# Kernel tuning notes

Hardware: AMD Instinct MI355X
Metric: run time of the kernel (lower is better)

Reference implementation:

```python
import jax, jax.numpy as jnp
import numpy as np

N = 16      # manifold_dim
H = 128     # hidden_dim
B = 256     # batch
EPS = 1e-6


def setup_inputs() -> dict:
    key = jax.random.key(0)
    ks = jax.random.split(key, 14)
    def w(k, shape):
        fan_in = shape[0]
        return jax.random.uniform(k, shape, jnp.float32, -1.0, 1.0) / np.sqrt(fan_in)
    return {
        "points": jax.random.normal(ks[0], (B, N), jnp.float32),
        # metric network: N -> H -> N*N
        "mW1": w(ks[1], (N, H)), "mb1": jnp.zeros((H,), jnp.float32),
        "mW2": w(ks[2], (H, N * N)), "mb2": jnp.zeros((N * N,), jnp.float32),
        # christoffel network: 3 -> H -> 1
        "cW1": w(ks[3], (3, H)), "cb1": jnp.zeros((H,), jnp.float32),
        "cW2": w(ks[4], (H, 1)), "cb2": jnp.zeros((1,), jnp.float32),
        # ricci network: 4N -> 2H -> N*N
        "rW1": w(ks[5], (4 * N, 2 * H)), "rb1": jnp.zeros((2 * H,), jnp.float32),
        "rW2": w(ks[6], (2 * H, N * N)), "rb2": jnp.zeros((N * N,), jnp.float32),
    }


def reference(points, mW1, mb1, mW2, mb2, cW1, cb1, cW2, cb2, rW1, rb1, rW2, rb2):
    b = points.shape[0]
    n = N
    # ---- metric: (b, n, n) ----
    mh = jax.nn.relu(points @ mW1 + mb1)
    metric = (mh @ mW2 + mb2).reshape(b, n, n)
    metric = metric + EPS * jnp.eye(n, dtype=metric.dtype)
    metric = 0.5 * (metric + jnp.swapaxes(metric, -2, -1))

    # ---- christoffel: vectorized over all (i,j,k) triples ----
    # inputs per triple: [metric_ij, metric_jk, metric_ki]
    m_ij = jnp.broadcast_to(metric[:, :, :, None], (b, n, n, n))
    m_jk = jnp.broadcast_to(metric[:, None, :, :], (b, n, n, n))
    mT = jnp.swapaxes(metric, -2, -1)  # mT[b,i,k] = metric[b,k,i]
    m_ki = jnp.broadcast_to(mT[:, :, None, :], (b, n, n, n))
    ch_in = jnp.stack([m_ij, m_jk, m_ki], axis=-1)        # (b,n,n,n,3)
    ch_h = jnp.tanh(ch_in @ cW1 + cb1)                    # (b,n,n,n,H)
    christoffel = (ch_h @ cW2 + cb2)[..., 0]              # (b,n,n,n)

    # ---- ricci: vectorized over all (i,j) pairs ----
    p_b = jnp.broadcast_to(points[:, None, None, :], (b, n, n, n))
    m_i = jnp.broadcast_to(metric[:, :, None, :], (b, n, n, n))
    m_j = jnp.broadcast_to(metric[:, None, :, :], (b, n, n, n))
    r_in = jnp.concatenate([p_b, m_i, m_j, christoffel], axis=-1)  # (b,n,n,4n)
    r_h = jax.nn.relu(r_in @ rW1 + rb1)                   # (b,n,n,2H)
    r_out = (r_h @ rW2 + rb2).reshape(b, n, n, n, n)      # (b,i,j,n,n)
    r_out = 0.5 * (r_out + jnp.swapaxes(r_out, -1, -2))
    ricci = r_out.sum(axis=(1, 2)) / (n * n)              # (b,n,n)
    return ricci
```

## Files before the change

kernel.cpp:

```cpp
#include <hip/hip_runtime.h>
#include <hip/hip_bf16.h>

#define NDIM 16
#define HDIM 128
#define BATCH 256
#define EPS_D 1e-6f

__global__ __launch_bounds__(256) void metric_proj_kernel(
    const float* __restrict__ points,
    const float* __restrict__ mW1, const float* __restrict__ mb1,
    const float* __restrict__ mW2, const float* __restrict__ mb2,
    const float* __restrict__ rW1, const float* __restrict__ rb1,
    float* __restrict__ metric,
    float* __restrict__ A1, float* __restrict__ Mi, float* __restrict__ Mj,
    float* __restrict__ G) {
  int b = blockIdx.x;
  int t = threadIdx.x;
  __shared__ float p[16];
  __shared__ float mh[128];
  __shared__ float raw[256];
  __shared__ float M[256];
  G[b * 256 + t] = 0.f;
  if (t < 16) p[t] = points[b * 16 + t];
  __syncthreads();
  if (t < 128) {
    float acc = mb1[t];
#pragma unroll
    for (int k = 0; k < 16; ++k) acc = fmaf(p[k], mW1[k * 128 + t], acc);
    mh[t] = fmaxf(acc, 0.f);
  }
  __syncthreads();
  {
    float acc = mb2[t];
#pragma unroll 8
    for (int h = 0; h < 128; ++h) acc = fmaf(mh[h], mW2[h * 256 + t], acc);
    raw[t] = acc;
  }
  __syncthreads();
  {
    int i = t >> 4, j = t & 15;
    float v = 0.5f * (raw[i * 16 + j] + raw[j * 16 + i]);
    if (i == j) v += EPS_D;
    M[t] = v;
    metric[b * 256 + t] = v;
  }
  __syncthreads();
  {
    int h = t;
    float wB[16], wC[16];
#pragma unroll
    for (int c = 0; c < 16; ++c) {
      wB[c] = rW1[(16 + c) * 256 + h];
      wC[c] = rW1[(32 + c) * 256 + h];
    }
    float a = rb1[h];
#pragma unroll
    for (int r = 0; r < 16; ++r) a = fmaf(p[r], rW1[r * 256 + h], a);
    A1[b * 256 + h] = a;
#pragma unroll 2
    for (int i = 0; i < 16; ++i) {
      float mi = 0.f, mj = 0.f;
#pragma unroll
      for (int c = 0; c < 16; ++c) {
        float m = M[i * 16 + c];
        mi = fmaf(m, wB[c], mi);
        mj = fmaf(m, wC[c], mj);
      }
      Mi[(b * 16 + i) * 256 + h] = mi;
      Mj[(b * 16 + i) * 256 + h] = mj;
    }
  }
}

__global__ __launch_bounds__(256, 4) void chr_kernel(
    const float* __restrict__ metric,
    const float* __restrict__ cW1, const float* __restrict__ cb1,
    const float* __restrict__ cW2, const float* __restrict__ cb2,
    const float* __restrict__ rW1,
    const float* __restrict__ A1, const float* __restrict__ Mi,
    const float* __restrict__ Mj,
    float* __restrict__ G) {
  int blk = blockIdx.x;
  int b = blk >> 2, g = blk & 3;
  int t = threadIdx.x;
  int w = t >> 6, l = t & 63;
  int i = g * 4 + w;
  int bi = b * 16 + i;
  __shared__ float M[256];
  __shared__ float4 z[128];
  __shared__ float4 w2p[32];
  __shared__ float4 ch4[256];
  float* chf = (float*)ch4;
  M[t] = metric[b * 256 + t];
  if (t < 128) {
    const float S = 2.8853900817779268f;
    z[t] = make_float4(S * cW1[t], S * cW1[128 + t], S * cW1[256 + t],
                       S * cb1[t]);
  } else {
    ((float*)w2p)[t - 128] = cW2[t - 128];
  }
  __syncthreads();

  {
    float x0[4], x1[4], x2[4], acc[4];
    float c2 = cb2[0];
#pragma unroll
    for (int m = 0; m < 4; ++m) {
      int jk = l + 64 * m;
      int j = jk >> 4, k = jk & 15;
      x0[m] = M[i * 16 + j];
      x1[m] = M[j * 16 + k];
      x2[m] = M[k * 16 + i];
      acc[m] = c2;
    }
    for (int h = 0; h < 128; h += 4) {
      float4 W2 = w2p[h >> 2];
      float w2u[4] = {W2.x, W2.y, W2.z, W2.w};
#pragma unroll
      for (int u = 0; u < 4; ++u) {
        float4 Q = z[h + u];
#pragma unroll
        for (int m = 0; m < 4; ++m) {
          float pre = fmaf(x0[m], Q.x, fmaf(x1[m], Q.y, fmaf(x2[m], Q.z, Q.w)));
          float e = __builtin_amdgcn_exp2f(pre);
          float r = __builtin_amdgcn_rcpf(e + 1.f);
          acc[m] = fmaf(w2u[u], fmaf(-2.f, r, 1.f), acc[m]);
        }
      }
    }
#pragma unroll
    for (int m = 0; m < 4; ++m) chf[w * 256 + l + 64 * m] = acc[m];
  }

  {
    float rc[4][16];
#pragma unroll
    for (int kk = 0; kk < 16; ++kk) {
#pragma unroll
      for (int m = 0; m < 4; ++m)
        rc[m][kk] = rW1[(48 + kk) * 256 + l + 64 * m];
    }
    float base[4], hacc[4];
#pragma unroll
    for (int m = 0; m < 4; ++m) {
      int h = l + 64 * m;
      base[m] = A1[b * 256 + h] + Mi[bi * 256 + h];
      hacc[m] = 0.f;
    }
    for (int jj = 0; jj < 16; ++jj) {
      float4 c0 = ch4[w * 64 + jj * 4 + 0];
      float4 c1 = ch4[w * 64 + jj * 4 + 1];
      float4 c2v = ch4[w * 64 + jj * 4 + 2];
      float4 c3 = ch4[w * 64 + jj * 4 + 3];
      float cc[16] = {c0.x, c0.y, c0.z, c0.w, c1.x, c1.y, c1.z, c1.w,
                      c2v.x, c2v.y, c2v.z, c2v.w, c3.x, c3.y, c3.z, c3.w};
#pragma unroll
      for (int m = 0; m < 4; ++m) {
        float cp = 0.f;
#pragma unroll
        for (int kk = 0; kk < 16; ++kk) cp = fmaf(cc[kk], rc[m][kk], cp);
        float mj = Mj[(b * 16 + jj) * 256 + l + 64 * m];
        hacc[m] += fmaxf(base[m] + mj + cp, 0.f);
      }
    }
#pragma unroll
    for (int m = 0; m < 4; ++m)
      atomicAdd(&G[b * 256 + l + 64 * m], hacc[m]);
  }
}

__global__ __launch_bounds__(256) void final_kernel(
    const float* __restrict__ G,
    const float* __restrict__ rW2, const float* __restrict__ rb2,
    float* __restrict__ out) {
  int b = blockIdx.x;
  int t = threadIdx.x;
  __shared__ float4 Gs[64];
  __shared__ float T[256];
  if (t < 64) Gs[t] = ((const float4*)(G + b * 256))[t];
  __syncthreads();
  float acc = 256.f * rb2[t];
#pragma unroll 4
  for (int h4 = 0; h4 < 64; ++h4) {
    float4 gg = Gs[h4];
    acc = fmaf(gg.x, rW2[(h4 * 4 + 0) * 256 + t], acc);
    acc = fmaf(gg.y, rW2[(h4 * 4 + 1) * 256 + t], acc);
    acc = fmaf(gg.z, rW2[(h4 * 4 + 2) * 256 + t], acc);
    acc = fmaf(gg.w, rW2[(h4 * 4 + 3) * 256 + t], acc);
  }
  T[t] = acc * (1.f / 256.f);
  __syncthreads();
  int k = t >> 4, lcol = t & 15;
  out[b * 256 + t] = 0.5f * (T[k * 16 + lcol] + T[lcol * 16 + k]);
}

extern "C" void kernel_launch(void* const* d_in, const int* in_sizes, int n_in,
                              void* d_out, int out_size, void* d_ws, size_t ws_size,
                              hipStream_t stream) {
  const float* points = (const float*)d_in[0];
  const float* mW1 = (const float*)d_in[1];
  const float* mb1 = (const float*)d_in[2];
  const float* mW2 = (const float*)d_in[3];
  const float* mb2 = (const float*)d_in[4];
  const float* cW1 = (const float*)d_in[5];
  const float* cb1 = (const float*)d_in[6];
  const float* cW2 = (const float*)d_in[7];
  const float* cb2 = (const float*)d_in[8];
  const float* rW1 = (const float*)d_in[9];
  const float* rb1 = (const float*)d_in[10];
  const float* rW2 = (const float*)d_in[11];
  const float* rb2 = (const float*)d_in[12];
  float* out = (float*)d_out;

  float* ws = (float*)d_ws;
  float* metric = ws;
  float* A1 = metric + 65536;
  float* Mi = A1 + 65536;
  float* Mj = Mi + 1048576;
  float* G = Mj + 1048576;

  metric_proj_kernel<<<BATCH, 256, 0, stream>>>(points, mW1, mb1, mW2, mb2,
                                                rW1, rb1, metric, A1, Mi, Mj, G);
  chr_kernel<<<BATCH * 4, 256, 0, stream>>>(metric, cW1, cb1, cW2, cb2, rW1,
                                            A1, Mi, Mj, G);
  final_kernel<<<BATCH, 256, 0, stream>>>(G, rW2, rb2, out);
}
```

Measured before the change: 143.6 us.

## Split christoffel kernel to one block per (b,i) with packed float2 math

Changes chr_kernel from 1024 blocks of 256 threads (4 i-rows each) to 4096 blocks of 128 threads, each handling one (b,i) row with two elements per thread. The arithmetic uses float2 vector types so the compiler can emit packed FMA instructions, while exp2 and rcp stay scalar. The aim is more parallel blocks, less per-thread register pressure and higher FMA throughput. In exchange the shared-memory weight setup is redone per block four times as often, and there are four times as many atomic adds to G.

```diff
diff --git a/kernel.cpp b/kernel.cpp
--- a/kernel.cpp
+++ b/kernel.cpp
@@ -5,6 +5,14 @@
 #define HDIM 128
 #define BATCH 256
 #define EPS_D 1e-6f
+
+typedef float v2f __attribute__((ext_vector_type(2)));
+static __device__ __forceinline__ v2f v2(float a, float b) {
+  v2f r; r.x = a; r.y = b; return r;
+}
+static __device__ __forceinline__ v2f splat(float a) {
+  v2f r; r.x = a; r.y = a; return r;
+}
 
 __global__ __launch_bounds__(256) void metric_proj_kernel(
     const float* __restrict__ points,
@@ -72,7 +80,7 @@
   }
 }
 
-__global__ __launch_bounds__(256, 4) void chr_kernel(
+__global__ __launch_bounds__(128, 6) void chr_kernel(
     const float* __restrict__ metric,
     const float* __restrict__ cW1, const float* __restrict__ cb1,
     const float* __restrict__ cW2, const float* __restrict__ cb2,
@@ -80,92 +88,88 @@
     const float* __restrict__ A1, const float* __restrict__ Mi,
     const float* __restrict__ Mj,
     float* __restrict__ G) {
-  int blk = blockIdx.x;
-  int b = blk >> 2, g = blk & 3;
+  int bi = blockIdx.x;
+  int b = bi >> 4, i = bi & 15;
   int t = threadIdx.x;
   int w = t >> 6, l = t & 63;
-  int i = g * 4 + w;
-  int bi = b * 16 + i;
   __shared__ float M[256];
   __shared__ float4 z[128];
   __shared__ float4 w2p[32];
-  __shared__ float4 ch4[256];
+  __shared__ float4 ch4[64];
   float* chf = (float*)ch4;
   M[t] = metric[b * 256 + t];
-  if (t < 128) {
+  M[t + 128] = metric[b * 256 + t + 128];
+  {
     const float S = 2.8853900817779268f;
     z[t] = make_float4(S * cW1[t], S * cW1[128 + t], S * cW1[256 + t],
                        S * cb1[t]);
-  } else {
-    ((float*)w2p)[t - 128] = cW2[t - 128];
-  }
-  __syncthreads();
-
-  {
-    float x0[4], x1[4], x2[4], acc[4];
-    float c2 = cb2[0];
-#pragma unroll
-    for (int m = 0; m < 4; ++m) {
-      int jk = l + 64 * m;
-      int j = jk >> 4, k = jk & 15;
-      x0[m] = M[i * 16 + j];
-      x1[m] = M[j * 16 + k];
-      x2[m] = M[k * 16 + i];
-      acc[m] = c2;
-    }
-    for (int h = 0; h < 128; h += 4) {
-      float4 W2 = w2p[h >> 2];
+    ((float*)w2p)[t] = cW2[t];
+  }
+  __syncthreads();
+
+  {
+    int jk0 = w * 128 + l, jk1 = jk0 + 64;
+    int j0 = jk0 >> 4, k0 = jk0 & 15;
+    int j1 = jk1 >> 4, k1 = jk1 & 15;
+    v2f x0 = v2(M[i * 16 + j0], M[i * 16 + j1]);
+    v2f x1 = v2(M[j0 * 16 + k0], M[j1 * 16 + k1]);
+    v2f x2 = v2(M[k0 * 16 + i], M[k1 * 16 + i]);
+    v2f acc = splat(cb2[0]);
+    for (int hq = 0; hq < 32; ++hq) {
+      float4 W2 = w2p[hq];
       float w2u[4] = {W2.x, W2.y, W2.z, W2.w};
 #pragma unroll
       for (int u = 0; u < 4; ++u) {
-        float4 Q = z[h + u];
-#pragma unroll
-        for (int m = 0; m < 4; ++m) {
-          float pre = fmaf(x0[m], Q.x, fmaf(x1[m], Q.y, fmaf(x2[m], Q.z, Q.w)));
-          float e = __builtin_amdgcn_exp2f(pre);
-          float r = __builtin_amdgcn_rcpf(e + 1.f);
-          acc[m] = fmaf(w2u[u], fmaf(-2.f, r, 1.f), acc[m]);
-        }
+        float4 Q = z[hq * 4 + u];
+        v2f pre = __builtin_elementwise_fma(
+            x0, splat(Q.x),
+            __builtin_elementwise_fma(
+                x1, splat(Q.y),
+                __builtin_elementwise_fma(x2, splat(Q.z), splat(Q.w))));
+        v2f e;
+        e.x = __builtin_amdgcn_exp2f(pre.x);
+        e.y = __builtin_amdgcn_exp2f(pre.y);
+        v2f ep = e + splat(1.f);
+        v2f r;
+        r.x = __builtin_amdgcn_rcpf(ep.x);
+        r.y = __builtin_amdgcn_rcpf(ep.y);
+        v2f th = __builtin_elementwise_fma(splat(-2.f), r, splat(1.f));
+        acc = __builtin_elementwise_fma(th, splat(w2u[u]), acc);
       }
     }
-#pragma unroll
-    for (int m = 0; m < 4; ++m) chf[w * 256 + l + 64 * m] = acc[m];
-  }
-
-  {
-    float rc[4][16];
-#pragma unroll
-    for (int kk = 0; kk < 16; ++kk) {
-#pragma unroll
-      for (int m = 0; m < 4; ++m)
-        rc[m][kk] = rW1[(48 + kk) * 256 + l + 64 * m];
-    }
-    float base[4], hacc[4];
-#pragma unroll
-    for (int m = 0; m < 4; ++m) {
-      int h = l + 64 * m;
-      base[m] = A1[b * 256 + h] + Mi[bi * 256 + h];
-      hacc[m] = 0.f;
-    }
+    chf[jk0] = acc.x;
+    chf[jk1] = acc.y;
+  }
+  __syncthreads();
+
+  {
+    int h0 = w * 128 + l, h1 = h0 + 64;
+    v2f rc2[16];
+#pragma unroll
+    for (int kk = 0; kk < 16; ++kk)
+      rc2[kk] = v2(rW1[(48 + kk) * 256 + h0], rW1[(48 + kk) * 256 + h1]);
+    v2f base = v2(A1[b * 256 + h0] + Mi[bi * 256 + h0],
+                  A1[b * 256 + h1] + Mi[bi * 256 + h1]);
+    v2f hacc = splat(0.f);
     for (int jj = 0; jj < 16; ++jj) {
-      float4 c0 = ch4[w * 64 + jj * 4 + 0];
-      float4 c1 = ch4[w * 64 + jj * 4 + 1];
-      float4 c2v = ch4[w * 64 + jj * 4 + 2];
-      float4 c3 = ch4[w * 64 + jj * 4 + 3];
+      float4 c0 = ch4[jj * 4 + 0];
+      float4 c1 = ch4[jj * 4 + 1];
+      float4 c2v = ch4[jj * 4 + 2];
+      float4 c3 = ch4[jj * 4 + 3];
+      v2f mj = v2(Mj[(b * 16 + jj) * 256 + h0], Mj[(b * 16 + jj) * 256 + h1]);
+      v2f cp = base + mj;
       float cc[16] = {c0.x, c0.y, c0.z, c0.w, c1.x, c1.y, c1.z, c1.w,
                       c2v.x, c2v.y, c2v.z, c2v.w, c3.x, c3.y, c3.z, c3.w};
 #pragma unroll
-      for (int m = 0; m < 4; ++m) {
-        float cp = 0.f;
-#pragma unroll
-        for (int kk = 0; kk < 16; ++kk) cp = fmaf(cc[kk], rc[m][kk], cp);
-        float mj = Mj[(b * 16 + jj) * 256 + l + 64 * m];
-        hacc[m] += fmaxf(base[m] + mj + cp, 0.f);
-      }
-    }
-#pragma unroll
-    for (int m = 0; m < 4; ++m)
-      atomicAdd(&G[b * 256 + l + 64 * m], hacc[m]);
+      for (int kk = 0; kk < 16; ++kk)
+        cp = __builtin_elementwise_fma(splat(cc[kk]), rc2[kk], cp);
+      v2f rl;
+      rl.x = fmaxf(cp.x, 0.f);
+      rl.y = fmaxf(cp.y, 0.f);
+      hacc += rl;
+    }
+    atomicAdd(&G[b * 256 + h0], hacc.x);
+    atomicAdd(&G[b * 256 + h1], hacc.y);
   }
 }
 
@@ -221,7 +225,7 @@
 
   metric_proj_kernel<<<BATCH, 256, 0, stream>>>(points, mW1, mb1, mW2, mb2,
                                                 rW1, rb1, metric, A1, Mi, Mj, G);
-  chr_kernel<<<BATCH * 4, 256, 0, stream>>>(metric, cW1, cb1, cW2, cb2, rW1,
-                                            A1, Mi, Mj, G);
+  chr_kernel<<<BATCH * NDIM, 128, 0, stream>>>(metric, cW1, cb1, cW2, cb2, rW1,
+                                               A1, Mi, Mj, G);
   final_kernel<<<BATCH, 256, 0, stream>>>(G, rW2, rb2, out);
 }
```

Result: faster. 135.7 us (-5.5%).

## Replace exp/rcp tanh with packed rational polynomial and vectorize via v2f packed FMA

Applied to the files above, without the earlier changes.

The christoffel hidden-layer tanh, previously computed with exp2 plus reciprocal, becomes a clamped odd rational polynomial evaluated with two-wide float vectors so the compiler can emit packed FP32 FMA instructions. The four per-lane denominators are inverted with a single reciprocal using a shared-product trick. The ricci first-layer accumulation is also rewritten with packed FMAs. The aim is to cut transcendental-unit work and halve the VALU instruction count, at the cost of more FMAs per element and slightly different tanh accuracy near the clamp.

```diff
diff --git a/kernel.cpp b/kernel.cpp
--- a/kernel.cpp
+++ b/kernel.cpp
@@ -5,6 +5,30 @@
 #define HDIM 128
 #define BATCH 256
 #define EPS_D 1e-6f
+
+typedef float v2f __attribute__((ext_vector_type(2)));
+static __device__ __forceinline__ v2f v2(float a, float b) {
+  v2f r; r.x = a; r.y = b; return r;
+}
+static __device__ __forceinline__ v2f splat(float a) {
+  v2f r; r.x = a; r.y = a; return r;
+}
+#define VFMA(a, b, c) __builtin_elementwise_fma((a), (b), (c))
+#define VMIN(a, b) __builtin_elementwise_min((a), (b))
+#define VMAX(a, b) __builtin_elementwise_max((a), (b))
+
+#define TCLAMP 7.99881172180175781f
+#define CA1 4.89352455891786e-03f
+#define CA3 6.37261928875436e-04f
+#define CA5 1.48572235717979e-05f
+#define CA7 5.12229709037114e-08f
+#define CA9 -8.60467152213735e-11f
+#define CA11 2.00018790482477e-13f
+#define CA13 -2.76076847742355e-16f
+#define CB0 4.89352518554385e-03f
+#define CB2 2.26843463243900e-03f
+#define CB4 1.18534705686654e-04f
+#define CB6 1.19825839466702e-06f
 
 __global__ __launch_bounds__(256) void metric_proj_kernel(
     const float* __restrict__ points,
@@ -88,65 +112,75 @@
   int bi = b * 16 + i;
   __shared__ float M[256];
   __shared__ float4 z[128];
-  __shared__ float4 w2p[32];
+  __shared__ float w2s[128];
   __shared__ float4 ch4[256];
   float* chf = (float*)ch4;
   M[t] = metric[b * 256 + t];
   if (t < 128) {
-    const float S = 2.8853900817779268f;
-    z[t] = make_float4(S * cW1[t], S * cW1[128 + t], S * cW1[256 + t],
-                       S * cb1[t]);
-  } else {
-    ((float*)w2p)[t - 128] = cW2[t - 128];
-  }
-  __syncthreads();
-
-  {
-    float x0[4], x1[4], x2[4], acc[4];
+    z[t] = make_float4(cW1[t], cW1[128 + t], cW1[256 + t], cb1[t]);
+    w2s[t] = cW2[t];
+  }
+  __syncthreads();
+
+  {
+    int j0 = l >> 4, k0 = l & 15;
+    v2f x0A = v2(M[i * 16 + j0], M[i * 16 + j0 + 8]);
+    v2f x0B = v2(M[i * 16 + j0 + 4], M[i * 16 + j0 + 12]);
+    v2f x1A = v2(M[j0 * 16 + k0], M[(j0 + 8) * 16 + k0]);
+    v2f x1B = v2(M[(j0 + 4) * 16 + k0], M[(j0 + 12) * 16 + k0]);
+    float x2s = M[k0 * 16 + i];
     float c2 = cb2[0];
-#pragma unroll
-    for (int m = 0; m < 4; ++m) {
-      int jk = l + 64 * m;
-      int j = jk >> 4, k = jk & 15;
-      x0[m] = M[i * 16 + j];
-      x1[m] = M[j * 16 + k];
-      x2[m] = M[k * 16 + i];
-      acc[m] = c2;
-    }
-    for (int h = 0; h < 128; h += 4) {
-      float4 W2 = w2p[h >> 2];
-      float w2u[4] = {W2.x, W2.y, W2.z, W2.w};
-#pragma unroll
-      for (int u = 0; u < 4; ++u) {
-        float4 Q = z[h + u];
-#pragma unroll
-        for (int m = 0; m < 4; ++m) {
-          float pre = fmaf(x0[m], Q.x, fmaf(x1[m], Q.y, fmaf(x2[m], Q.z, Q.w)));
-          float e = __builtin_amdgcn_exp2f(pre);
-          float r = __builtin_amdgcn_rcpf(e + 1.f);
-          acc[m] = fmaf(w2u[u], fmaf(-2.f, r, 1.f), acc[m]);
-        }
-      }
-    }
-#pragma unroll
-    for (int m = 0; m < 4; ++m) chf[w * 256 + l + 64 * m] = acc[m];
-  }
-
-  {
-    float rc[4][16];
+    v2f accA = splat(c2), accB = splat(c2);
+#pragma unroll 2
+    for (int h = 0; h < 128; ++h) {
+      float4 Q = z[h];
+      float w2h = w2s[h];
+      float bb = fmaf(x2s, Q.z, Q.w);
+      v2f preA = VFMA(x0A, splat(Q.x), VFMA(x1A, splat(Q.y), splat(bb)));
+      v2f preB = VFMA(x0B, splat(Q.x), VFMA(x1B, splat(Q.y), splat(bb)));
+      v2f tA = VMAX(VMIN(preA, splat(TCLAMP)), splat(-TCLAMP));
+      v2f tB = VMAX(VMIN(preB, splat(TCLAMP)), splat(-TCLAMP));
+      v2f sA = tA * tA, sB = tB * tB;
+      v2f pA = VFMA(sA, splat(CA13), splat(CA11));
+      v2f pB = VFMA(sB, splat(CA13), splat(CA11));
+      pA = VFMA(sA, pA, splat(CA9));  pB = VFMA(sB, pB, splat(CA9));
+      pA = VFMA(sA, pA, splat(CA7));  pB = VFMA(sB, pB, splat(CA7));
+      pA = VFMA(sA, pA, splat(CA5));  pB = VFMA(sB, pB, splat(CA5));
+      pA = VFMA(sA, pA, splat(CA3));  pB = VFMA(sB, pB, splat(CA3));
+      pA = VFMA(sA, pA, splat(CA1));  pB = VFMA(sB, pB, splat(CA1));
+      pA = pA * tA;  pB = pB * tB;
+      v2f qA = VFMA(sA, splat(CB6), splat(CB4));
+      v2f qB = VFMA(sB, splat(CB6), splat(CB4));
+      qA = VFMA(sA, qA, splat(CB2));  qB = VFMA(sB, qB, splat(CB2));
+      qA = VFMA(sA, qA, splat(CB0));  qB = VFMA(sB, qB, splat(CB0));
+      v2f prod = qA * qB;
+      float r = __builtin_amdgcn_rcpf(prod.x * prod.y);
+      v2f u = splat(r) * v2(prod.y, prod.x);
+      v2f rcpA = u * qB;
+      v2f rcpB = u * qA;
+      accA = VFMA(pA * rcpA, splat(w2h), accA);
+      accB = VFMA(pB * rcpB, splat(w2h), accB);
+    }
+    chf[w * 256 + l] = accA.x;
+    chf[w * 256 + l + 64] = accB.x;
+    chf[w * 256 + l + 128] = accA.y;
+    chf[w * 256 + l + 192] = accB.y;
+  }
+
+  {
+    int h0 = l, h1 = l + 64, h2 = l + 128, h3 = l + 192;
+    v2f rcA[16], rcB[16];
 #pragma unroll
     for (int kk = 0; kk < 16; ++kk) {
-#pragma unroll
-      for (int m = 0; m < 4; ++m)
-        rc[m][kk] = rW1[(48 + kk) * 256 + l + 64 * m];
-    }
-    float base[4], hacc[4];
-#pragma unroll
-    for (int m = 0; m < 4; ++m) {
-      int h = l + 64 * m;
-      base[m] = A1[b * 256 + h] + Mi[bi * 256 + h];
-      hacc[m] = 0.f;
-    }
+      const float* row = rW1 + (48 + kk) * 256;
+      rcA[kk] = v2(row[h0], row[h2]);
+      rcB[kk] = v2(row[h1], row[h3]);
+    }
+    const float* A1b = A1 + b * 256;
+    const float* Mib = Mi + bi * 256;
+    v2f baseA = v2(A1b[h0] + Mib[h0], A1b[h2] + Mib[h2]);
+    v2f baseB = v2(A1b[h1] + Mib[h1], A1b[h3] + Mib[h3]);
+    v2f haccA = splat(0.f), haccB = splat(0.f);
     for (int jj = 0; jj < 16; ++jj) {
       float4 c0 = ch4[w * 64 + jj * 4 + 0];
       float4 c1 = ch4[w * 64 + jj * 4 + 1];
@@ -154,18 +188,21 @@
       float4 c3 = ch4[w * 64 + jj * 4 + 3];
       float cc[16] = {c0.x, c0.y, c0.z, c0.w, c1.x, c1.y, c1.z, c1.w,
                       c2v.x, c2v.y, c2v.z, c2v.w, c3.x, c3.y, c3.z, c3.w};
-#pragma unroll
-      for (int m = 0; m < 4; ++m) {
-        float cp = 0.f;
-#pragma unroll
-        for (int kk = 0; kk < 16; ++kk) cp = fmaf(cc[kk], rc[m][kk], cp);
-        float mj = Mj[(b * 16 + jj) * 256 + l + 64 * m];
-        hacc[m] += fmaxf(base[m] + mj + cp, 0.f);
+      const float* Mjr = Mj + (b * 16 + jj) * 256;
+      v2f cpA = baseA + v2(Mjr[h0], Mjr[h2]);
+      v2f cpB = baseB + v2(Mjr[h1], Mjr[h3]);
+#pragma unroll
+      for (int kk = 0; kk < 16; ++kk) {
+        cpA = VFMA(splat(cc[kk]), rcA[kk], cpA);
+        cpB = VFMA(splat(cc[kk]), rcB[kk], cpB);
       }
-    }
-#pragma unroll
-    for (int m = 0; m < 4; ++m)
-      atomicAdd(&G[b * 256 + l + 64 * m], hacc[m]);
+      haccA += VMAX(cpA, splat(0.f));
+      haccB += VMAX(cpB, splat(0.f));
+    }
+    atomicAdd(&G[b * 256 + h0], haccA.x);
+    atomicAdd(&G[b * 256 + h1], haccB.x);
+    atomicAdd(&G[b * 256 + h2], haccA.y);
+    atomicAdd(&G[b * 256 + h3], haccB.y);
   }
 }
 
```

Measured after the change: 158.1 us. 10.1% more time.
